# Kernel optimization log

Measured on AMD Instinct MI355X. Metric: run time of the kernel, lower is better.

## Reference

```python
import jax, jax.numpy as jnp
import numpy as np

SEQ = 32
D = 32  # d_model == GRU hidden size


def _gru_scan(gates_x, w_hh, b_hh):
    """gates_x: [S, B, 3H] precomputed input projections (r,z,n order, PyTorch convention).
    Returns outputs [S, B, H]."""
    H = w_hh.shape[1]
    B = gates_x.shape[1]

    def step(h, gx):
        gh = h @ w_hh.T + b_hh  # [B, 3H]
        r = jax.nn.sigmoid(gx[:, :H] + gh[:, :H])
        z = jax.nn.sigmoid(gx[:, H:2 * H] + gh[:, H:2 * H])
        n = jnp.tanh(gx[:, 2 * H:] + r * gh[:, 2 * H:])
        h_new = (1.0 - z) * n + z * h
        return h_new, h_new

    h0 = jnp.zeros((B, H), gates_x.dtype)
    _, ys = jax.lax.scan(step, h0, gates_x)
    return ys


def setup_inputs() -> dict:
    key = jax.random.key(0)
    ks = jax.random.split(key, 16)
    s = 0.1
    inp = {
        "x": jax.random.normal(ks[0], (32768, SEQ), dtype=jnp.float32),
        # feature extractor: Linear(1,16) -> LeakyReLU -> Linear(16,32)
        "w1": jax.random.normal(ks[1], (16, 1), dtype=jnp.float32) * s,
        "b1": jax.random.normal(ks[2], (16,), dtype=jnp.float32) * s,
        "w2": jax.random.normal(ks[3], (D, 16), dtype=jnp.float32) * s,
        "b2": jax.random.normal(ks[4], (D,), dtype=jnp.float32) * s,
        # GRU forward direction (PyTorch layout: [3H, in], gates r,z,n)
        "w_ih_f": jax.random.normal(ks[5], (3 * D, D), dtype=jnp.float32) * s,
        "w_hh_f": jax.random.normal(ks[6], (3 * D, D), dtype=jnp.float32) * s,
        "b_ih_f": jax.random.normal(ks[7], (3 * D,), dtype=jnp.float32) * s,
        "b_hh_f": jax.random.normal(ks[8], (3 * D,), dtype=jnp.float32) * s,
        # GRU backward direction
        "w_ih_b": jax.random.normal(ks[9], (3 * D, D), dtype=jnp.float32) * s,
        "w_hh_b": jax.random.normal(ks[10], (3 * D, D), dtype=jnp.float32) * s,
        "b_ih_b": jax.random.normal(ks[11], (3 * D,), dtype=jnp.float32) * s,
        "b_hh_b": jax.random.normal(ks[12], (3 * D,), dtype=jnp.float32) * s,
        # decoder: Linear(2*D, 128)
        "w_dec": jax.random.normal(ks[13], (128, 2 * D), dtype=jnp.float32) * s,
        "b_dec": jax.random.normal(ks[14], (128,), dtype=jnp.float32) * s,
    }
    return inp


def reference(x, w1, b1, w2, b2,
              w_ih_f, w_hh_f, b_ih_f, b_hh_f,
              w_ih_b, w_hh_b, b_ih_b, b_hh_b,
              w_dec, b_dec):
    x = x.reshape(-1, SEQ, 1)                      # [B, S, 1]
    h = jax.nn.leaky_relu(x @ w1.T + b1, 0.01)     # [B, S, 16]
    feat = h @ w2.T + b2                           # [B, S, D]

    # forward direction
    gx_f = jnp.einsum('bsd,gd->sbg', feat, w_ih_f) + b_ih_f  # [S, B, 3D]
    out_f = _gru_scan(gx_f, w_hh_f, b_hh_f)                  # [S, B, D]

    # backward direction: scan over time-reversed input, flip outputs back
    feat_rev = feat[:, ::-1, :]
    gx_b = jnp.einsum('bsd,gd->sbg', feat_rev, w_ih_b) + b_ih_b
    out_b = _gru_scan(gx_b, w_hh_b, b_hh_b)[::-1]            # [S, B, D]

    out = jnp.concatenate([out_f, out_b], axis=-1)  # [S, B, 2D]
    pooled = out.mean(axis=0)                       # [B, 2D]
    return pooled @ w_dec.T + b_dec                 # [B, 128]
```

## Files before the change

### kernel.cpp

```cpp
#include <hip/hip_runtime.h>


#define SEQB 32
#define NH   16
#define DH   32

typedef __attribute__((ext_vector_type(4))) float f32x4;
typedef __attribute__((ext_vector_type(8))) short s16x8;
typedef __attribute__((ext_vector_type(4))) unsigned int u32x4;

#define MFMA_B16(a, b, c) __builtin_amdgcn_mfma_f32_16x16x32_bf16((a), (b), (c), 0, 0, 0)

#define OFF_AHI  0u
#define OFF_ALO  12288u
#define OFF_AGX  24576u
#define OFF_ADEC 36864u
#define OFF_WC   53248u
#define OFF_BC   65536u

__device__ __forceinline__ unsigned short bf16_rne(float x) {
    unsigned u = __float_as_uint(x);
    return (unsigned short)((u + 0x7fffu + ((u >> 16) & 1u)) >> 16);
}
__device__ __forceinline__ unsigned pack_hi(unsigned a, unsigned b) {
    return __builtin_amdgcn_perm(a, b, 0x07060302u);
}
__device__ __forceinline__ int kperm(int q, int e) {
    return (e < 4) ? (4 * q + e) : (4 * q + 12 + e);
}

__global__ __launch_bounds__(1024) void gru_precompute_kernel(
    const float* __restrict__ w_ih_f, const float* __restrict__ b_ih_f,
    const float* __restrict__ w_ih_b, const float* __restrict__ b_ih_b,
    const float* __restrict__ w2, const float* __restrict__ b2,
    const float* __restrict__ whh_f, const float* __restrict__ whh_b,
    const float* __restrict__ bhh_f, const float* __restrict__ bhh_b,
    const float* __restrict__ w_dec,
    unsigned char* __restrict__ ws)
{
    const int t = threadIdx.x;
    float* WC = (float*)(ws + OFF_WC);
    float* BC = (float*)(ws + OFF_BC);

    if (t < 192) {
        const int dir = t / 96, g = t % 96;
        const float* wih = dir ? w_ih_b : w_ih_f;
        const float* bih = dir ? b_ih_b : b_ih_f;
        float acc[NH];
#pragma unroll
        for (int m = 0; m < NH; ++m) acc[m] = 0.0f;
        float ab = bih[g];
        for (int d = 0; d < DH; ++d) {
            float wv = wih[g * DH + d];
            ab = fmaf(wv, b2[d], ab);
#pragma unroll
            for (int m = 0; m < NH; ++m) acc[m] = fmaf(wv, w2[d * NH + m], acc[m]);
        }
#pragma unroll
        for (int m = 0; m < NH; ++m) WC[(dir * 96 + g) * NH + m] = acc[m];
        BC[dir * 96 + g] = ab;
    }
    __syncthreads();

    if (t < 768) {
        const int dir = t / 384, r = t % 384, tt = r / 64, l = r % 64;
        const int gate = tt * 16 + (l & 15);
        const int q = l >> 4;
        const float* whh = dir ? whh_b : whh_f;
        const float* bhh = dir ? bhh_b : bhh_f;
        unsigned short h8[8], l8[8], g8[8];
#pragma unroll
        for (int e = 0; e < 8; ++e) {
            const int u = kperm(q, e);
            float w = whh[gate * DH + u];
            unsigned ub = __float_as_uint(w);
            h8[e] = (unsigned short)(ub >> 16);
            l8[e] = bf16_rne(w - __uint_as_float(ub & 0xffff0000u));
            float gxv = (e < 4) ? WC[(dir * 96 + gate) * NH + 4 * q + e] : 0.0f;
            g8[e] = bf16_rne(gxv);
        }
        const float bias = BC[dir * 96 + gate] + ((gate < 64) ? bhh[gate] : 0.0f);
        const unsigned bb = __float_as_uint(bias);
        if (q == 0) g8[4] = (unsigned short)(bb >> 16);
        if (q == 1) g8[4] = bf16_rne(bias - __uint_as_float(bb & 0xffff0000u));

        unsigned short* dh = (unsigned short*)(ws + OFF_AHI + dir * 6144u + tt * 1024u + l * 16u);
        unsigned short* dl = (unsigned short*)(ws + OFF_ALO + dir * 6144u + tt * 1024u + l * 16u);
        unsigned short* dg = (unsigned short*)(ws + OFF_AGX + dir * 6144u + tt * 1024u + l * 16u);
#pragma unroll
        for (int e = 0; e < 8; ++e) { dh[e] = h8[e]; dl[e] = l8[e]; dg[e] = g8[e]; }
    }
    {
        const int kc = t / 512, r = t % 512, tt = r / 64, l = r % 64;
        const int outn = tt * 16 + (l & 15);
        const int q = l >> 4;
        unsigned short* dd = (unsigned short*)(ws + OFF_ADEC + kc * 8192u + tt * 1024u + l * 16u);
#pragma unroll
        for (int e = 0; e < 8; ++e)
            dd[e] = bf16_rne(w_dec[outn * 64 + kperm(q, e) + 32 * kc]);
    }
}

__global__ __launch_bounds__(64, 2) void gru_mfma_kernel(
    const float* __restrict__ x,
    const float* __restrict__ w1, const float* __restrict__ b1,
    const float* __restrict__ bhh_f, const float* __restrict__ bhh_b,
    const unsigned char* __restrict__ ws,
    const float* __restrict__ b_dec,
    float* __restrict__ out)
{
    const int l = threadIdx.x;
    const int n = l & 15;
    const int q = l >> 4;
    const int rowbase = blockIdx.x * 16;
    const float* xr = x + (size_t)(rowbase + n) * SEQB;

    const float4 w1q = *(const float4*)(w1 + 4 * q);
    const float4 b1q = *(const float4*)(b1 + 4 * q);

    float pFL[4], pFH[4], pBL[4], pBH[4];

#pragma unroll 1
    for (int dir = 0; dir < 2; ++dir) {
        const float* bhh = dir ? bhh_b : bhh_f;
        const unsigned char* pAhi = ws + OFF_AHI + dir * 6144u + l * 16u;
        const unsigned char* pAlo = ws + OFF_ALO + dir * 6144u + l * 16u;
        const unsigned char* pAgx = ws + OFF_AGX + dir * 6144u + l * 16u;
        s16x8 Ahi[6], Alo[6], Agx[6];
#pragma unroll
        for (int tt = 0; tt < 6; ++tt) {
            Ahi[tt] = *(const s16x8*)(pAhi + tt * 1024);
            Alo[tt] = *(const s16x8*)(pAlo + tt * 1024);
            Agx[tt] = *(const s16x8*)(pAgx + tt * 1024);
        }
#pragma unroll
        for (int tt = 0; tt < 6; ++tt)
            asm volatile("" : "+v"(Ahi[tt]), "+v"(Alo[tt]), "+v"(Agx[tt]));
        const float4 bn0f = *(const float4*)(bhh + 64 + 4 * q);
        const float4 bn1f = *(const float4*)(bhh + 80 + 4 * q);
        const f32x4 bhn0 = {bn0f.x, bn0f.y, bn0f.z, bn0f.w};
        const f32x4 bhn1 = {bn1f.x, bn1f.y, bn1f.z, bn1f.w};

        float hL[4] = {0, 0, 0, 0}, hH[4] = {0, 0, 0, 0};
        float pL[4] = {0, 0, 0, 0}, pH[4] = {0, 0, 0, 0};

#pragma unroll 1
        for (int blk = 0; blk < 4; ++blk) {
            const int bb = dir ? 3 - blk : blk;
            const float4 xa = *(const float4*)(xr + bb * 8);
            const float4 xb = *(const float4*)(xr + bb * 8 + 4);
            const float raw[8] = {xa.x, xa.y, xa.z, xa.w, xb.x, xb.y, xb.z, xb.w};
            float xs[8];
#pragma unroll
            for (int i = 0; i < 8; ++i) xs[i] = dir ? raw[7 - i] : raw[i];

#pragma unroll
            for (int i = 0; i < 8; ++i) {
                float t0 = fmaf(xs[i], w1q.x, b1q.x); t0 = fmaxf(t0, 0.01f * t0);
                float t1 = fmaf(xs[i], w1q.y, b1q.y); t1 = fmaxf(t1, 0.01f * t1);
                float t2 = fmaf(xs[i], w1q.z, b1q.z); t2 = fmaxf(t2, 0.01f * t2);
                float t3 = fmaf(xs[i], w1q.w, b1q.w); t3 = fmaxf(t3, 0.01f * t3);
                u32x4 ub1;
                ub1.x = pack_hi(__float_as_uint(t1), __float_as_uint(t0));
                ub1.y = pack_hi(__float_as_uint(t3), __float_as_uint(t2));
                ub1.z = 0x00003F80u;
                ub1.w = 0u;
                const s16x8 Bh1 = __builtin_bit_cast(s16x8, ub1);

                unsigned uL0 = __float_as_uint(hL[0]), uL1 = __float_as_uint(hL[1]);
                unsigned uL2 = __float_as_uint(hL[2]), uL3 = __float_as_uint(hL[3]);
                unsigned uH0 = __float_as_uint(hH[0]), uH1 = __float_as_uint(hH[1]);
                unsigned uH2 = __float_as_uint(hH[2]), uH3 = __float_as_uint(hH[3]);
                u32x4 phh;
                phh.x = pack_hi(uL1, uL0); phh.y = pack_hi(uL3, uL2);
                phh.z = pack_hi(uH1, uH0); phh.w = pack_hi(uH3, uH2);
                float lL0 = hL[0] - __uint_as_float(uL0 & 0xffff0000u);
                float lL1 = hL[1] - __uint_as_float(uL1 & 0xffff0000u);
                float lL2 = hL[2] - __uint_as_float(uL2 & 0xffff0000u);
                float lL3 = hL[3] - __uint_as_float(uL3 & 0xffff0000u);
                float lH0 = hH[0] - __uint_as_float(uH0 & 0xffff0000u);
                float lH1 = hH[1] - __uint_as_float(uH1 & 0xffff0000u);
                float lH2 = hH[2] - __uint_as_float(uH2 & 0xffff0000u);
                float lH3 = hH[3] - __uint_as_float(uH3 & 0xffff0000u);
                u32x4 phl;
                phl.x = pack_hi(__float_as_uint(lL1), __float_as_uint(lL0));
                phl.y = pack_hi(__float_as_uint(lL3), __float_as_uint(lL2));
                phl.z = pack_hi(__float_as_uint(lH1), __float_as_uint(lH0));
                phl.w = pack_hi(__float_as_uint(lH3), __float_as_uint(lH2));
                const s16x8 Bhhi = __builtin_bit_cast(s16x8, phh);
                const s16x8 Bhlo = __builtin_bit_cast(s16x8, phl);

                const f32x4 z4 = {0.0f, 0.0f, 0.0f, 0.0f};
                f32x4 a0 = MFMA_B16(Agx[0], Bh1, z4);
                a0 = MFMA_B16(Alo[0], Bhhi, a0); a0 = MFMA_B16(Ahi[0], Bhlo, a0); a0 = MFMA_B16(Ahi[0], Bhhi, a0);
                f32x4 a1 = MFMA_B16(Agx[1], Bh1, z4);
                a1 = MFMA_B16(Alo[1], Bhhi, a1); a1 = MFMA_B16(Ahi[1], Bhlo, a1); a1 = MFMA_B16(Ahi[1], Bhhi, a1);
                f32x4 a2 = MFMA_B16(Agx[2], Bh1, z4);
                a2 = MFMA_B16(Alo[2], Bhhi, a2); a2 = MFMA_B16(Ahi[2], Bhlo, a2); a2 = MFMA_B16(Ahi[2], Bhhi, a2);
                f32x4 a3 = MFMA_B16(Agx[3], Bh1, z4);
                a3 = MFMA_B16(Alo[3], Bhhi, a3); a3 = MFMA_B16(Ahi[3], Bhlo, a3); a3 = MFMA_B16(Ahi[3], Bhhi, a3);
                f32x4 x4a = MFMA_B16(Agx[4], Bh1, z4);
                f32x4 x5a = MFMA_B16(Agx[5], Bh1, z4);
                f32x4 g4 = MFMA_B16(Alo[4], Bhhi, bhn0);
                g4 = MFMA_B16(Ahi[4], Bhlo, g4); g4 = MFMA_B16(Ahi[4], Bhhi, g4);
                f32x4 g5 = MFMA_B16(Alo[5], Bhhi, bhn1);
                g5 = MFMA_B16(Ahi[5], Bhlo, g5); g5 = MFMA_B16(Ahi[5], Bhhi, g5);

#pragma unroll
                for (int rg = 0; rg < 4; ++rg) {
                    float rL = __builtin_amdgcn_rcpf(1.0f + __expf(-a0[rg]));
                    float zL = __builtin_amdgcn_rcpf(1.0f + __expf(-a2[rg]));
                    float tL = fmaf(rL, g4[rg], x4a[rg]);
                    float nL = fmaf(-2.0f, __builtin_amdgcn_rcpf(1.0f + __expf(tL + tL)), 1.0f);
                    hL[rg] = fmaf(zL, hL[rg] - nL, nL);
                    pL[rg] += hL[rg];

                    float rH = __builtin_amdgcn_rcpf(1.0f + __expf(-a1[rg]));
                    float zH = __builtin_amdgcn_rcpf(1.0f + __expf(-a3[rg]));
                    float tH = fmaf(rH, g5[rg], x5a[rg]);
                    float nH = fmaf(-2.0f, __builtin_amdgcn_rcpf(1.0f + __expf(tH + tH)), 1.0f);
                    hH[rg] = fmaf(zH, hH[rg] - nH, nH);
                    pH[rg] += hH[rg];
                }
            }
        }
        if (dir == 0) {
#pragma unroll
            for (int rg = 0; rg < 4; ++rg) { pFL[rg] = pL[rg]; pFH[rg] = pH[rg]; }
        } else {
#pragma unroll
            for (int rg = 0; rg < 4; ++rg) { pBL[rg] = pL[rg]; pBH[rg] = pH[rg]; }
        }
    }

    {
#pragma unroll
        for (int rg = 0; rg < 4; ++rg) {
            pFL[rg] *= 0.03125f; pFH[rg] *= 0.03125f;
            pBL[rg] *= 0.03125f; pBH[rg] *= 0.03125f;
        }
        u32x4 pfh, pfl, pbh, pbl;
        unsigned v0, v1, v2, v3;
        v0 = __float_as_uint(pFL[0]); v1 = __float_as_uint(pFL[1]);
        v2 = __float_as_uint(pFL[2]); v3 = __float_as_uint(pFL[3]);
        pfh.x = pack_hi(v1, v0); pfh.y = pack_hi(v3, v2);
        pfl.x = pack_hi(__float_as_uint(pFL[1] - __uint_as_float(v1 & 0xffff0000u)),
                        __float_as_uint(pFL[0] - __uint_as_float(v0 & 0xffff0000u)));
        pfl.y = pack_hi(__float_as_uint(pFL[3] - __uint_as_float(v3 & 0xffff0000u)),
                        __float_as_uint(pFL[2] - __uint_as_float(v2 & 0xffff0000u)));
        v0 = __float_as_uint(pFH[0]); v1 = __float_as_uint(pFH[1]);
        v2 = __float_as_uint(pFH[2]); v3 = __float_as_uint(pFH[3]);
        pfh.z = pack_hi(v1, v0); pfh.w = pack_hi(v3, v2);
        pfl.z = pack_hi(__float_as_uint(pFH[1] - __uint_as_float(v1 & 0xffff0000u)),
                        __float_as_uint(pFH[0] - __uint_as_float(v0 & 0xffff0000u)));
        pfl.w = pack_hi(__float_as_uint(pFH[3] - __uint_as_float(v3 & 0xffff0000u)),
                        __float_as_uint(pFH[2] - __uint_as_float(v2 & 0xffff0000u)));
        v0 = __float_as_uint(pBL[0]); v1 = __float_as_uint(pBL[1]);
        v2 = __float_as_uint(pBL[2]); v3 = __float_as_uint(pBL[3]);
        pbh.x = pack_hi(v1, v0); pbh.y = pack_hi(v3, v2);
        pbl.x = pack_hi(__float_as_uint(pBL[1] - __uint_as_float(v1 & 0xffff0000u)),
                        __float_as_uint(pBL[0] - __uint_as_float(v0 & 0xffff0000u)));
        pbl.y = pack_hi(__float_as_uint(pBL[3] - __uint_as_float(v3 & 0xffff0000u)),
                        __float_as_uint(pBL[2] - __uint_as_float(v2 & 0xffff0000u)));
        v0 = __float_as_uint(pBH[0]); v1 = __float_as_uint(pBH[1]);
        v2 = __float_as_uint(pBH[2]); v3 = __float_as_uint(pBH[3]);
        pbh.z = pack_hi(v1, v0); pbh.w = pack_hi(v3, v2);
        pbl.z = pack_hi(__float_as_uint(pBH[1] - __uint_as_float(v1 & 0xffff0000u)),
                        __float_as_uint(pBH[0] - __uint_as_float(v0 & 0xffff0000u)));
        pbl.w = pack_hi(__float_as_uint(pBH[3] - __uint_as_float(v3 & 0xffff0000u)),
                        __float_as_uint(pBH[2] - __uint_as_float(v2 & 0xffff0000u)));
        const s16x8 BpFh = __builtin_bit_cast(s16x8, pfh);
        const s16x8 BpFl = __builtin_bit_cast(s16x8, pfl);
        const s16x8 BpBh = __builtin_bit_cast(s16x8, pbh);
        const s16x8 BpBl = __builtin_bit_cast(s16x8, pbl);

#pragma unroll
        for (int tt = 0; tt < 8; ++tt) {
            const s16x8 A0 = *(const s16x8*)(ws + OFF_ADEC + tt * 1024u + l * 16u);
            const s16x8 A1 = *(const s16x8*)(ws + OFF_ADEC + 8192u + tt * 1024u + l * 16u);
            const float4 bd = *(const float4*)(b_dec + tt * 16 + 4 * q);
            f32x4 acc = {bd.x, bd.y, bd.z, bd.w};
            acc = MFMA_B16(A0, BpFl, acc);
            acc = MFMA_B16(A1, BpBl, acc);
            acc = MFMA_B16(A0, BpFh, acc);
            acc = MFMA_B16(A1, BpBh, acc);
            *(float4*)(out + (size_t)(rowbase + n) * 128 + tt * 16 + 4 * q) =
                make_float4(acc[0], acc[1], acc[2], acc[3]);
        }
    }
}

extern "C" void kernel_launch(void* const* d_in, const int* in_sizes, int n_in,
                              void* d_out, int out_size, void* d_ws, size_t ws_size,
                              hipStream_t stream)
{
    const float* x    = (const float*)d_in[0];
    const float* w1   = (const float*)d_in[1];
    const float* b1   = (const float*)d_in[2];
    const float* w2   = (const float*)d_in[3];
    const float* b2   = (const float*)d_in[4];
    const float* wihf = (const float*)d_in[5];
    const float* whhf = (const float*)d_in[6];
    const float* bihf = (const float*)d_in[7];
    const float* bhhf = (const float*)d_in[8];
    const float* wihb = (const float*)d_in[9];
    const float* whhb = (const float*)d_in[10];
    const float* bihb = (const float*)d_in[11];
    const float* bhhb = (const float*)d_in[12];
    const float* wdec = (const float*)d_in[13];
    const float* bdec = (const float*)d_in[14];
    float* out = (float*)d_out;
    unsigned char* ws = (unsigned char*)d_ws;

    const int B = in_sizes[0] / SEQB;
    const int grid = B / 16;

    hipLaunchKernelGGL(gru_precompute_kernel, dim3(1), dim3(1024), 0, stream,
                       wihf, bihf, wihb, bihb, w2, b2, whhf, whhb, bhhf, bhhb, wdec, ws);
    hipLaunchKernelGGL(gru_mfma_kernel, dim3(grid), dim3(64), 0, stream,
                       x, w1, b1, bhhf, bhhb, ws, bdec, out);
}
```

Before: 82.59 us.

## Interleave forward/backward GRU recurrences and drop low-part W_hh split

Runs the forward and backward GRU directions interleaved in one time loop instead of sequentially, so two independent dependency chains overlap MFMA and transcendental latency. It also drops the low-order bf16 correction term of the recurrent weights, rounding W_hh to a single bf16 and removing one MFMA per gate tile per step. The cost is more live registers (both directions' weights and states), which may cause spilling at the 64-thread/2-wave launch bounds, and reduced precision of the recurrent matmul.

Measured after the change: 138.8 us. +68.0%, slower.

```diff
diff --git a/kernel.cpp b/kernel.cpp
--- a/kernel.cpp
+++ b/kernel.cpp
@@ -12,7 +12,6 @@
 #define MFMA_B16(a, b, c) __builtin_amdgcn_mfma_f32_16x16x32_bf16((a), (b), (c), 0, 0, 0)
 
 #define OFF_AHI  0u
-#define OFF_ALO  12288u
 #define OFF_AGX  24576u
 #define OFF_ADEC 36864u
 #define OFF_WC   53248u
@@ -68,14 +67,11 @@
         const int q = l >> 4;
         const float* whh = dir ? whh_b : whh_f;
         const float* bhh = dir ? bhh_b : bhh_f;
-        unsigned short h8[8], l8[8], g8[8];
+        unsigned short h8[8], g8[8];
 #pragma unroll
         for (int e = 0; e < 8; ++e) {
             const int u = kperm(q, e);
-            float w = whh[gate * DH + u];
-            unsigned ub = __float_as_uint(w);
-            h8[e] = (unsigned short)(ub >> 16);
-            l8[e] = bf16_rne(w - __uint_as_float(ub & 0xffff0000u));
+            h8[e] = bf16_rne(whh[gate * DH + u]);
             float gxv = (e < 4) ? WC[(dir * 96 + gate) * NH + 4 * q + e] : 0.0f;
             g8[e] = bf16_rne(gxv);
         }
@@ -85,10 +81,9 @@
         if (q == 1) g8[4] = bf16_rne(bias - __uint_as_float(bb & 0xffff0000u));
 
         unsigned short* dh = (unsigned short*)(ws + OFF_AHI + dir * 6144u + tt * 1024u + l * 16u);
-        unsigned short* dl = (unsigned short*)(ws + OFF_ALO + dir * 6144u + tt * 1024u + l * 16u);
         unsigned short* dg = (unsigned short*)(ws + OFF_AGX + dir * 6144u + tt * 1024u + l * 16u);
 #pragma unroll
-        for (int e = 0; e < 8; ++e) { dh[e] = h8[e]; dl[e] = l8[e]; dg[e] = g8[e]; }
+        for (int e = 0; e < 8; ++e) { dh[e] = h8[e]; dg[e] = g8[e]; }
     }
     {
         const int kc = t / 512, r = t % 512, tt = r / 64, l = r % 64;
@@ -98,6 +93,80 @@
 #pragma unroll
         for (int e = 0; e < 8; ++e)
             dd[e] = bf16_rne(w_dec[outn * 64 + kperm(q, e) + 32 * kc]);
+    }
+}
+
+__device__ __forceinline__ void gru_step(
+    float xs, const float4& w1q, const float4& b1q,
+    const s16x8* Ahi, const s16x8* Agx,
+    const f32x4& bhn0, const f32x4& bhn1,
+    float hL[4], float hH[4], float pL[4], float pH[4])
+{
+    float t0 = fmaf(xs, w1q.x, b1q.x); t0 = fmaxf(t0, 0.01f * t0);
+    float t1 = fmaf(xs, w1q.y, b1q.y); t1 = fmaxf(t1, 0.01f * t1);
+    float t2 = fmaf(xs, w1q.z, b1q.z); t2 = fmaxf(t2, 0.01f * t2);
+    float t3 = fmaf(xs, w1q.w, b1q.w); t3 = fmaxf(t3, 0.01f * t3);
+    u32x4 ub1;
+    ub1.x = pack_hi(__float_as_uint(t1), __float_as_uint(t0));
+    ub1.y = pack_hi(__float_as_uint(t3), __float_as_uint(t2));
+    ub1.z = 0x00003F80u;
+    ub1.w = 0u;
+    const s16x8 Bh1 = __builtin_bit_cast(s16x8, ub1);
+
+    unsigned uL0 = __float_as_uint(hL[0]), uL1 = __float_as_uint(hL[1]);
+    unsigned uL2 = __float_as_uint(hL[2]), uL3 = __float_as_uint(hL[3]);
+    unsigned uH0 = __float_as_uint(hH[0]), uH1 = __float_as_uint(hH[1]);
+    unsigned uH2 = __float_as_uint(hH[2]), uH3 = __float_as_uint(hH[3]);
+    u32x4 phh;
+    phh.x = pack_hi(uL1, uL0); phh.y = pack_hi(uL3, uL2);
+    phh.z = pack_hi(uH1, uH0); phh.w = pack_hi(uH3, uH2);
+    float lL0 = hL[0] - __uint_as_float(uL0 & 0xffff0000u);
+    float lL1 = hL[1] - __uint_as_float(uL1 & 0xffff0000u);
+    float lL2 = hL[2] - __uint_as_float(uL2 & 0xffff0000u);
+    float lL3 = hL[3] - __uint_as_float(uL3 & 0xffff0000u);
+    float lH0 = hH[0] - __uint_as_float(uH0 & 0xffff0000u);
+    float lH1 = hH[1] - __uint_as_float(uH1 & 0xffff0000u);
+    float lH2 = hH[2] - __uint_as_float(uH2 & 0xffff0000u);
+    float lH3 = hH[3] - __uint_as_float(uH3 & 0xffff0000u);
+    u32x4 phl;
+    phl.x = pack_hi(__float_as_uint(lL1), __float_as_uint(lL0));
+    phl.y = pack_hi(__float_as_uint(lL3), __float_as_uint(lL2));
+    phl.z = pack_hi(__float_as_uint(lH1), __float_as_uint(lH0));
+    phl.w = pack_hi(__float_as_uint(lH3), __float_as_uint(lH2));
+    const s16x8 Bhhi = __builtin_bit_cast(s16x8, phh);
+    const s16x8 Bhlo = __builtin_bit_cast(s16x8, phl);
+
+    const f32x4 z4 = {0.0f, 0.0f, 0.0f, 0.0f};
+    f32x4 a0 = MFMA_B16(Agx[0], Bh1, z4);
+    a0 = MFMA_B16(Ahi[0], Bhlo, a0); a0 = MFMA_B16(Ahi[0], Bhhi, a0);
+    f32x4 a1 = MFMA_B16(Agx[1], Bh1, z4);
+    a1 = MFMA_B16(Ahi[1], Bhlo, a1); a1 = MFMA_B16(Ahi[1], Bhhi, a1);
+    f32x4 a2 = MFMA_B16(Agx[2], Bh1, z4);
+    a2 = MFMA_B16(Ahi[2], Bhlo, a2); a2 = MFMA_B16(Ahi[2], Bhhi, a2);
+    f32x4 a3 = MFMA_B16(Agx[3], Bh1, z4);
+    a3 = MFMA_B16(Ahi[3], Bhlo, a3); a3 = MFMA_B16(Ahi[3], Bhhi, a3);
+    f32x4 x4a = MFMA_B16(Agx[4], Bh1, z4);
+    f32x4 x5a = MFMA_B16(Agx[5], Bh1, z4);
+    f32x4 g4 = MFMA_B16(Ahi[4], Bhlo, bhn0);
+    g4 = MFMA_B16(Ahi[4], Bhhi, g4);
+    f32x4 g5 = MFMA_B16(Ahi[5], Bhlo, bhn1);
+    g5 = MFMA_B16(Ahi[5], Bhhi, g5);
+
+#pragma unroll
+    for (int rg = 0; rg < 4; ++rg) {
+        float rL = __builtin_amdgcn_rcpf(1.0f + __expf(-a0[rg]));
+        float zL = __builtin_amdgcn_rcpf(1.0f + __expf(-a2[rg]));
+        float tL = fmaf(rL, g4[rg], x4a[rg]);
+        float nL = fmaf(-2.0f, __builtin_amdgcn_rcpf(1.0f + __expf(tL + tL)), 1.0f);
+        hL[rg] = fmaf(zL, hL[rg] - nL, nL);
+        pL[rg] += hL[rg];
+
+        float rH = __builtin_amdgcn_rcpf(1.0f + __expf(-a1[rg]));
+        float zH = __builtin_amdgcn_rcpf(1.0f + __expf(-a3[rg]));
+        float tH = fmaf(rH, g5[rg], x5a[rg]);
+        float nH = fmaf(-2.0f, __builtin_amdgcn_rcpf(1.0f + __expf(tH + tH)), 1.0f);
+        hH[rg] = fmaf(zH, hH[rg] - nH, nH);
+        pH[rg] += hH[rg];
     }
 }
 
@@ -118,157 +187,87 @@
     const float4 w1q = *(const float4*)(w1 + 4 * q);
     const float4 b1q = *(const float4*)(b1 + 4 * q);
 
-    float pFL[4], pFH[4], pBL[4], pBH[4];
+    s16x8 AhiF[6], AgxF[6], AhiB[6], AgxB[6];
+    {
+        const unsigned char* pHF = ws + OFF_AHI + l * 16u;
+        const unsigned char* pGF = ws + OFF_AGX + l * 16u;
+        const unsigned char* pHB = pHF + 6144u;
+        const unsigned char* pGB = pGF + 6144u;
+#pragma unroll
+        for (int tt = 0; tt < 6; ++tt) {
+            AhiF[tt] = *(const s16x8*)(pHF + tt * 1024);
+            AgxF[tt] = *(const s16x8*)(pGF + tt * 1024);
+            AhiB[tt] = *(const s16x8*)(pHB + tt * 1024);
+            AgxB[tt] = *(const s16x8*)(pGB + tt * 1024);
+        }
+#pragma unroll
+        for (int tt = 0; tt < 6; ++tt)
+            asm volatile("" : "+v"(AhiF[tt]), "+v"(AgxF[tt]), "+v"(AhiB[tt]), "+v"(AgxB[tt]));
+    }
+    const float4 bn0Ff = *(const float4*)(bhh_f + 64 + 4 * q);
+    const float4 bn1Ff = *(const float4*)(bhh_f + 80 + 4 * q);
+    const float4 bn0Bf = *(const float4*)(bhh_b + 64 + 4 * q);
+    const float4 bn1Bf = *(const float4*)(bhh_b + 80 + 4 * q);
+    const f32x4 bhn0F = {bn0Ff.x, bn0Ff.y, bn0Ff.z, bn0Ff.w};
+    const f32x4 bhn1F = {bn1Ff.x, bn1Ff.y, bn1Ff.z, bn1Ff.w};
+    const f32x4 bhn0B = {bn0Bf.x, bn0Bf.y, bn0Bf.z, bn0Bf.w};
+    const f32x4 bhn1B = {bn1Bf.x, bn1Bf.y, bn1Bf.z, bn1Bf.w};
+
+    float hLF[4] = {0,0,0,0}, hHF[4] = {0,0,0,0}, pLF[4] = {0,0,0,0}, pHF[4] = {0,0,0,0};
+    float hLB[4] = {0,0,0,0}, hHB[4] = {0,0,0,0}, pLB[4] = {0,0,0,0}, pHB[4] = {0,0,0,0};
 
 #pragma unroll 1
-    for (int dir = 0; dir < 2; ++dir) {
-        const float* bhh = dir ? bhh_b : bhh_f;
-        const unsigned char* pAhi = ws + OFF_AHI + dir * 6144u + l * 16u;
-        const unsigned char* pAlo = ws + OFF_ALO + dir * 6144u + l * 16u;
-        const unsigned char* pAgx = ws + OFF_AGX + dir * 6144u + l * 16u;
-        s16x8 Ahi[6], Alo[6], Agx[6];
-#pragma unroll
-        for (int tt = 0; tt < 6; ++tt) {
-            Ahi[tt] = *(const s16x8*)(pAhi + tt * 1024);
-            Alo[tt] = *(const s16x8*)(pAlo + tt * 1024);
-            Agx[tt] = *(const s16x8*)(pAgx + tt * 1024);
-        }
-#pragma unroll
-        for (int tt = 0; tt < 6; ++tt)
-            asm volatile("" : "+v"(Ahi[tt]), "+v"(Alo[tt]), "+v"(Agx[tt]));
-        const float4 bn0f = *(const float4*)(bhh + 64 + 4 * q);
-        const float4 bn1f = *(const float4*)(bhh + 80 + 4 * q);
-        const f32x4 bhn0 = {bn0f.x, bn0f.y, bn0f.z, bn0f.w};
-        const f32x4 bhn1 = {bn1f.x, bn1f.y, bn1f.z, bn1f.w};
-
-        float hL[4] = {0, 0, 0, 0}, hH[4] = {0, 0, 0, 0};
-        float pL[4] = {0, 0, 0, 0}, pH[4] = {0, 0, 0, 0};
-
-#pragma unroll 1
-        for (int blk = 0; blk < 4; ++blk) {
-            const int bb = dir ? 3 - blk : blk;
-            const float4 xa = *(const float4*)(xr + bb * 8);
-            const float4 xb = *(const float4*)(xr + bb * 8 + 4);
-            const float raw[8] = {xa.x, xa.y, xa.z, xa.w, xb.x, xb.y, xb.z, xb.w};
-            float xs[8];
-#pragma unroll
-            for (int i = 0; i < 8; ++i) xs[i] = dir ? raw[7 - i] : raw[i];
-
-#pragma unroll
-            for (int i = 0; i < 8; ++i) {
-                float t0 = fmaf(xs[i], w1q.x, b1q.x); t0 = fmaxf(t0, 0.01f * t0);
-                float t1 = fmaf(xs[i], w1q.y, b1q.y); t1 = fmaxf(t1, 0.01f * t1);
-                float t2 = fmaf(xs[i], w1q.z, b1q.z); t2 = fmaxf(t2, 0.01f * t2);
-                float t3 = fmaf(xs[i], w1q.w, b1q.w); t3 = fmaxf(t3, 0.01f * t3);
-                u32x4 ub1;
-                ub1.x = pack_hi(__float_as_uint(t1), __float_as_uint(t0));
-                ub1.y = pack_hi(__float_as_uint(t3), __float_as_uint(t2));
-                ub1.z = 0x00003F80u;
-                ub1.w = 0u;
-                const s16x8 Bh1 = __builtin_bit_cast(s16x8, ub1);
-
-                unsigned uL0 = __float_as_uint(hL[0]), uL1 = __float_as_uint(hL[1]);
-                unsigned uL2 = __float_as_uint(hL[2]), uL3 = __float_as_uint(hL[3]);
-                unsigned uH0 = __float_as_uint(hH[0]), uH1 = __float_as_uint(hH[1]);
-                unsigned uH2 = __float_as_uint(hH[2]), uH3 = __float_as_uint(hH[3]);
-                u32x4 phh;
-                phh.x = pack_hi(uL1, uL0); phh.y = pack_hi(uL3, uL2);
-                phh.z = pack_hi(uH1, uH0); phh.w = pack_hi(uH3, uH2);
-                float lL0 = hL[0] - __uint_as_float(uL0 & 0xffff0000u);
-                float lL1 = hL[1] - __uint_as_float(uL1 & 0xffff0000u);
-                float lL2 = hL[2] - __uint_as_float(uL2 & 0xffff0000u);
-                float lL3 = hL[3] - __uint_as_float(uL3 & 0xffff0000u);
-                float lH0 = hH[0] - __uint_as_float(uH0 & 0xffff0000u);
-                float lH1 = hH[1] - __uint_as_float(uH1 & 0xffff0000u);
-                float lH2 = hH[2] - __uint_as_float(uH2 & 0xffff0000u);
-                float lH3 = hH[3] - __uint_as_float(uH3 & 0xffff0000u);
-                u32x4 phl;
-                phl.x = pack_hi(__float_as_uint(lL1), __float_as_uint(lL0));
-                phl.y = pack_hi(__float_as_uint(lL3), __float_as_uint(lL2));
-                phl.z = pack_hi(__float_as_uint(lH1), __float_as_uint(lH0));
-                phl.w = pack_hi(__float_as_uint(lH3), __float_as_uint(lH2));
-                const s16x8 Bhhi = __builtin_bit_cast(s16x8, phh);
-                const s16x8 Bhlo = __builtin_bit_cast(s16x8, phl);
-
-                const f32x4 z4 = {0.0f, 0.0f, 0.0f, 0.0f};
-                f32x4 a0 = MFMA_B16(Agx[0], Bh1, z4);
-                a0 = MFMA_B16(Alo[0], Bhhi, a0); a0 = MFMA_B16(Ahi[0], Bhlo, a0); a0 = MFMA_B16(Ahi[0], Bhhi, a0);
-                f32x4 a1 = MFMA_B16(Agx[1], Bh1, z4);
-                a1 = MFMA_B16(Alo[1], Bhhi, a1); a1 = MFMA_B16(Ahi[1], Bhlo, a1); a1 = MFMA_B16(Ahi[1], Bhhi, a1);
-                f32x4 a2 = MFMA_B16(Agx[2], Bh1, z4);
-                a2 = MFMA_B16(Alo[2], Bhhi, a2); a2 = MFMA_B16(Ahi[2], Bhlo, a2); a2 = MFMA_B16(Ahi[2], Bhhi, a2);
-                f32x4 a3 = MFMA_B16(Agx[3], Bh1, z4);
-                a3 = MFMA_B16(Alo[3], Bhhi, a3); a3 = MFMA_B16(Ahi[3], Bhlo, a3); a3 = MFMA_B16(Ahi[3], Bhhi, a3);
-                f32x4 x4a = MFMA_B16(Agx[4], Bh1, z4);
-                f32x4 x5a = MFMA_B16(Agx[5], Bh1, z4);
-                f32x4 g4 = MFMA_B16(Alo[4], Bhhi, bhn0);
-                g4 = MFMA_B16(Ahi[4], Bhlo, g4); g4 = MFMA_B16(Ahi[4], Bhhi, g4);
-                f32x4 g5 = MFMA_B16(Alo[5], Bhhi, bhn1);
-                g5 = MFMA_B16(Ahi[5], Bhlo, g5); g5 = MFMA_B16(Ahi[5], Bhhi, g5);
-
-#pragma unroll
-                for (int rg = 0; rg < 4; ++rg) {
-                    float rL = __builtin_amdgcn_rcpf(1.0f + __expf(-a0[rg]));
-                    float zL = __builtin_amdgcn_rcpf(1.0f + __expf(-a2[rg]));
-                    float tL = fmaf(rL, g4[rg], x4a[rg]);
-                    float nL = fmaf(-2.0f, __builtin_amdgcn_rcpf(1.0f + __expf(tL + tL)), 1.0f);
-                    hL[rg] = fmaf(zL, hL[rg] - nL, nL);
-                    pL[rg] += hL[rg];
-
-                    float rH = __builtin_amdgcn_rcpf(1.0f + __expf(-a1[rg]));
-                    float zH = __builtin_amdgcn_rcpf(1.0f + __expf(-a3[rg]));
-                    float tH = fmaf(rH, g5[rg], x5a[rg]);
-                    float nH = fmaf(-2.0f, __builtin_amdgcn_rcpf(1.0f + __expf(tH + tH)), 1.0f);
-                    hH[rg] = fmaf(zH, hH[rg] - nH, nH);
-                    pH[rg] += hH[rg];
-                }
-            }
-        }
-        if (dir == 0) {
-#pragma unroll
-            for (int rg = 0; rg < 4; ++rg) { pFL[rg] = pL[rg]; pFH[rg] = pH[rg]; }
-        } else {
-#pragma unroll
-            for (int rg = 0; rg < 4; ++rg) { pBL[rg] = pL[rg]; pBH[rg] = pH[rg]; }
+    for (int blk = 0; blk < 4; ++blk) {
+        const float4 xa = *(const float4*)(xr + blk * 8);
+        const float4 xb = *(const float4*)(xr + blk * 8 + 4);
+        const float4 xc = *(const float4*)(xr + (3 - blk) * 8);
+        const float4 xd = *(const float4*)(xr + (3 - blk) * 8 + 4);
+        const float xF[8] = {xa.x, xa.y, xa.z, xa.w, xb.x, xb.y, xb.z, xb.w};
+        const float xB[8] = {xd.w, xd.z, xd.y, xd.x, xc.w, xc.z, xc.y, xc.x};
+
+#pragma unroll
+        for (int i = 0; i < 8; ++i) {
+            gru_step(xF[i], w1q, b1q, AhiF, AgxF, bhn0F, bhn1F, hLF, hHF, pLF, pHF);
+            gru_step(xB[i], w1q, b1q, AhiB, AgxB, bhn0B, bhn1B, hLB, hHB, pLB, pHB);
         }
     }
 
     {
 #pragma unroll
         for (int rg = 0; rg < 4; ++rg) {
-            pFL[rg] *= 0.03125f; pFH[rg] *= 0.03125f;
-            pBL[rg] *= 0.03125f; pBH[rg] *= 0.03125f;
+            pLF[rg] *= 0.03125f; pHF[rg] *= 0.03125f;
+            pLB[rg] *= 0.03125f; pHB[rg] *= 0.03125f;
         }
         u32x4 pfh, pfl, pbh, pbl;
         unsigned v0, v1, v2, v3;
-        v0 = __float_as_uint(pFL[0]); v1 = __float_as_uint(pFL[1]);
-        v2 = __float_as_uint(pFL[2]); v3 = __float_as_uint(pFL[3]);
+        v0 = __float_as_uint(pLF[0]); v1 = __float_as_uint(pLF[1]);
+        v2 = __float_as_uint(pLF[2]); v3 = __float_as_uint(pLF[3]);
         pfh.x = pack_hi(v1, v0); pfh.y = pack_hi(v3, v2);
-        pfl.x = pack_hi(__float_as_uint(pFL[1] - __uint_as_float(v1 & 0xffff0000u)),
-                        __float_as_uint(pFL[0] - __uint_as_float(v0 & 0xffff0000u)));
-        pfl.y = pack_hi(__float_as_uint(pFL[3] - __uint_as_float(v3 & 0xffff0000u)),
-                        __float_as_uint(pFL[2] - __uint_as_float(v2 & 0xffff0000u)));
-        v0 = __float_as_uint(pFH[0]); v1 = __float_as_uint(pFH[1]);
-        v2 = __float_as_uint(pFH[2]); v3 = __float_as_uint(pFH[3]);
+        pfl.x = pack_hi(__float_as_uint(pLF[1] - __uint_as_float(v1 & 0xffff0000u)),
+                        __float_as_uint(pLF[0] - __uint_as_float(v0 & 0xffff0000u)));
+        pfl.y = pack_hi(__float_as_uint(pLF[3] - __uint_as_float(v3 & 0xffff0000u)),
+                        __float_as_uint(pLF[2] - __uint_as_float(v2 & 0xffff0000u)));
+        v0 = __float_as_uint(pHF[0]); v1 = __float_as_uint(pHF[1]);
+        v2 = __float_as_uint(pHF[2]); v3 = __float_as_uint(pHF[3]);
         pfh.z = pack_hi(v1, v0); pfh.w = pack_hi(v3, v2);
-        pfl.z = pack_hi(__float_as_uint(pFH[1] - __uint_as_float(v1 & 0xffff0000u)),
-                        __float_as_uint(pFH[0] - __uint_as_float(v0 & 0xffff0000u)));
-        pfl.w = pack_hi(__float_as_uint(pFH[3] - __uint_as_float(v3 & 0xffff0000u)),
-                        __float_as_uint(pFH[2] - __uint_as_float(v2 & 0xffff0000u)));
-        v0 = __float_as_uint(pBL[0]); v1 = __float_as_uint(pBL[1]);
-        v2 = __float_as_uint(pBL[2]); v3 = __float_as_uint(pBL[3]);
+        pfl.z = pack_hi(__float_as_uint(pHF[1] - __uint_as_float(v1 & 0xffff0000u)),
+                        __float_as_uint(pHF[0] - __uint_as_float(v0 & 0xffff0000u)));
+        pfl.w = pack_hi(__float_as_uint(pHF[3] - __uint_as_float(v3 & 0xffff0000u)),
+                        __float_as_uint(pHF[2] - __uint_as_float(v2 & 0xffff0000u)));
+        v0 = __float_as_uint(pLB[0]); v1 = __float_as_uint(pLB[1]);
+        v2 = __float_as_uint(pLB[2]); v3 = __float_as_uint(pLB[3]);
         pbh.x = pack_hi(v1, v0); pbh.y = pack_hi(v3, v2);
-        pbl.x = pack_hi(__float_as_uint(pBL[1] - __uint_as_float(v1 & 0xffff0000u)),
-                        __float_as_uint(pBL[0] - __uint_as_float(v0 & 0xffff0000u)));
-        pbl.y = pack_hi(__float_as_uint(pBL[3] - __uint_as_float(v3 & 0xffff0000u)),
-                        __float_as_uint(pBL[2] - __uint_as_float(v2 & 0xffff0000u)));
-        v0 = __float_as_uint(pBH[0]); v1 = __float_as_uint(pBH[1]);
-        v2 = __float_as_uint(pBH[2]); v3 = __float_as_uint(pBH[3]);
+        pbl.x = pack_hi(__float_as_uint(pLB[1] - __uint_as_float(v1 & 0xffff0000u)),
+                        __float_as_uint(pLB[0] - __uint_as_float(v0 & 0xffff0000u)));
+        pbl.y = pack_hi(__float_as_uint(pLB[3] - __uint_as_float(v3 & 0xffff0000u)),
+                        __float_as_uint(pLB[2] - __uint_as_float(v2 & 0xffff0000u)));
+        v0 = __float_as_uint(pHB[0]); v1 = __float_as_uint(pHB[1]);
+        v2 = __float_as_uint(pHB[2]); v3 = __float_as_uint(pHB[3]);
         pbh.z = pack_hi(v1, v0); pbh.w = pack_hi(v3, v2);
-        pbl.z = pack_hi(__float_as_uint(pBH[1] - __uint_as_float(v1 & 0xffff0000u)),
-                        __float_as_uint(pBH[0] - __uint_as_float(v0 & 0xffff0000u)));
-        pbl.w = pack_hi(__float_as_uint(pBH[3] - __uint_as_float(v3 & 0xffff0000u)),
-                        __float_as_uint(pBH[2] - __uint_as_float(v2 & 0xffff0000u)));
+        pbl.z = pack_hi(__float_as_uint(pHB[1] - __uint_as_float(v1 & 0xffff0000u)),
+                        __float_as_uint(pHB[0] - __uint_as_float(v0 & 0xffff0000u)));
+        pbl.w = pack_hi(__float_as_uint(pHB[3] - __uint_as_float(v3 & 0xffff0000u)),
+                        __float_as_uint(pHB[2] - __uint_as_float(v2 & 0xffff0000u)));
         const s16x8 BpFh = __builtin_bit_cast(s16x8, pfh);
         const s16x8 BpFl = __builtin_bit_cast(s16x8, pfl);
         const s16x8 BpBh = __builtin_bit_cast(s16x8, pbh);
```
